# Kernel tuning notes

Hardware: AMD Instinct MI355X
Metric: run time of the kernel (lower is better)

## Reference

```python
import jax, jax.numpy as jnp
import numpy as np

NUM_LAYERS = 2      # args.num_layers
EPS = 1e-6          # poincare_to_lorentz eps
NORM_CLIP = 1.0     # exp_map norm_control clip
N, K, F, D = 30000, 32, 256, 128


def _normalize_lorentz(h):
    # project onto hyperboloid: time = sqrt(1 + |space|^2)
    sp = h[:, 1:]
    t = jnp.sqrt(1.0 + jnp.sum(sp * sp, axis=-1, keepdims=True))
    return jnp.concatenate([t, sp], axis=-1)


def _exp_map_zero(v):
    # tangent vector at origin has zero time component (normalize_tan with x=0)
    sp = v[:, 1:]
    ldv = jnp.sum(sp * sp, axis=-1, keepdims=True)          # Lorentz norm^2 of (0, sp)
    nd = jnp.sqrt(jnp.clip(ldv + 1e-9, 1e-10, None))
    t = jnp.minimum(nd, NORM_CLIP)                           # norm_control
    time = jnp.cosh(t)
    space = jnp.sinh(t) * sp / nd
    return _normalize_lorentz(jnp.concatenate([time, space], axis=-1))


def _hyperbolic_mean(nbr, w):
    # nbr: [N, K, D] Lorentz points; w: [N, K] neighbor weights
    k = nbr[..., 1:] / nbr[..., :1]                          # h2k: Klein model
    kn = jnp.clip(jnp.sum(k * k, axis=-1, keepdims=True), 0.0, 0.9)
    lam = w[..., None] / jnp.sqrt(1.0 - kn)                  # weighted Lorentz factors
    k_mean = jnp.sum(lam * k, axis=1) / jnp.sum(lam, axis=1)  # [N, D-1]
    # k2h: Klein -> hyperboloid
    kn2 = jnp.minimum(jnp.sum(k_mean * k_mean, axis=-1, keepdims=True), 0.9)
    ones = jnp.ones((k_mean.shape[0], 1), k_mean.dtype)
    return jnp.concatenate([ones, k_mean], axis=-1) / jnp.sqrt(1.0 - kn2)


def _lorentz_activation(h):
    # lorentz -> poincare, SELU, poincare -> lorentz (c = 1)
    p = h[:, 1:] / (h[:, :1] + 1.0)
    p = jax.nn.selu(p)
    pn = jnp.sum(p * p, axis=-1, keepdims=True)
    return jnp.concatenate([1.0 + pn, 2.0 * p], axis=-1) / (1.0 - pn + EPS)


def setup_inputs() -> dict:
    key = jax.random.key(0)
    k1, k2, k3, k4, k5 = jax.random.split(key, 5)
    x = jax.random.normal(k1, (N, F), dtype=jnp.float32)
    adj = jax.random.randint(k2, (N, K), 0, N, dtype=jnp.int32)
    w = jax.random.uniform(k3, (N, K), dtype=jnp.float32)
    lin_W = jax.random.normal(k4, (F, D), dtype=jnp.float32) / np.sqrt(F)
    lin_b = jnp.zeros((D,), dtype=jnp.float32)
    M, _ = jnp.linalg.qr(jax.random.normal(k5, (D - 1, D - 1), dtype=jnp.float32))  # orthogonal init
    return {"x": x, "adj": adj, "w": w, "lin_W": lin_W, "lin_b": lin_b, "M": M}


def reference(x, adj, w, lin_W, lin_b, M):
    h = jax.nn.selu(x @ lin_W + lin_b)          # Euclidean projection + activation
    h = _exp_map_zero(h)                        # lift to hyperboloid
    d = h.shape[-1]
    # retrieve_params: block-diag [[1,0],[0,M]] Lorentz rotation (tie_weight -> shared)
    lw = jnp.zeros((d, d), h.dtype).at[0, 0].set(1.0).at[1:, 1:].set(M)
    for _ in range(NUM_LAYERS):
        msg = h @ lw                             # Stiefel transform
        nbr = msg[adj]                           # [N, K, D] neighbor gather
        h = _hyperbolic_mean(nbr, w)             # Klein weighted mean
        h = _lorentz_activation(h)               # SELU in Poincare model
        h = _normalize_lorentz(h)                # re-project onto hyperboloid
    return h
```

## Files before the change

kernel.cpp:

```cpp
#include <hip/hip_runtime.h>
#include <hip/hip_fp16.h>
#include <math.h>

#define NN 30000
#define KK 32
#define FF 256
#define DD 128
#define NB 938

typedef _Float16 f16x8 __attribute__((ext_vector_type(8)));
typedef float f32x4v __attribute__((ext_vector_type(4)));

__device__ __forceinline__ float seluf(float x) {
    const float scale = 1.0507009873554804934193349852946f;
    const float alpha = 1.6732632423543772848170429916717f;
    return x > 0.f ? scale * x : scale * alpha * expm1f(x);
}

__device__ __forceinline__ float waveReduceSum(float v) {
#pragma unroll
    for (int m = 1; m < 64; m <<= 1) v += __shfl_xor(v, m, 64);
    return v;
}

__global__ __launch_bounds__(256) void k_prep(
    const float* __restrict__ W, const float* __restrict__ M,
    _Float16* __restrict__ Wt, _Float16* __restrict__ Lt)
{
    const int b = blockIdx.x, t = threadIdx.x;
    if (b < 128) {
        Wt[b * FF + t] = (_Float16)W[t * DD + b];
    } else if (t < 128) {
        const int c = b - 128, k = t;
        const float v = (k == 0 && c == 0) ? 1.f
                      : ((k >= 1 && c >= 1) ? M[(k - 1) * 127 + (c - 1)] : 0.f);
        Lt[c * DD + k] = (_Float16)v;
    }
}

__global__ __launch_bounds__(256) void k_lin_exp(
    const float* __restrict__ x, const _Float16* __restrict__ Wt,
    const float* __restrict__ b, float* __restrict__ h)
{
    __shared__ float red[4][16];
    const int wv_ = threadIdx.x >> 6;
    const int lane = threadIdx.x & 63;
    const int g = lane >> 4, c16 = lane & 15;
    const int baseRow = blockIdx.x * 32 + (wv_ >> 1) * 16;
    const int nb = (wv_ & 1) * 4;
    const int arow = baseRow + c16;
    const bool rowOK = arow < NN;

    float4 f[16];
    const float4* xp = (const float4*)(x + (size_t)arow * FF) + g * 2;
    if (rowOK) {
#pragma unroll
        for (int ks = 0; ks < 8; ++ks) {
            f[2 * ks]     = xp[ks * 8];
            f[2 * ks + 1] = xp[ks * 8 + 1];
        }
    } else {
#pragma unroll
        for (int i = 0; i < 16; ++i) f[i] = float4{0.f, 0.f, 0.f, 0.f};
    }
    f16x8 ahi[8], alo[8];
#pragma unroll
    for (int ks = 0; ks < 8; ++ks) {
        const float q[8] = {f[2 * ks].x, f[2 * ks].y, f[2 * ks].z, f[2 * ks].w,
                            f[2 * ks + 1].x, f[2 * ks + 1].y, f[2 * ks + 1].z, f[2 * ks + 1].w};
#pragma unroll
        for (int j = 0; j < 8; ++j) {
            ahi[ks][j] = (_Float16)q[j];
            alo[ks][j] = (_Float16)(q[j] - (float)ahi[ks][j]);
        }
    }

    f32x4v acc[4];
#pragma unroll
    for (int n = 0; n < 4; ++n) acc[n] = f32x4v{0.f, 0.f, 0.f, 0.f};
#pragma unroll
    for (int ks = 0; ks < 8; ++ks) {
#pragma unroll
        for (int n = 0; n < 4; ++n) {
            const f16x8 bh = *(const f16x8*)(Wt + (size_t)((nb + n) * 16 + c16) * FF + ks * 32 + g * 8);
            acc[n] = __builtin_amdgcn_mfma_f32_16x16x32_f16(ahi[ks], bh, acc[n], 0, 0, 0);
            acc[n] = __builtin_amdgcn_mfma_f32_16x16x32_f16(alo[ks], bh, acc[n], 0, 0, 0);
        }
    }

    float bias[4];
#pragma unroll
    for (int n = 0; n < 4; ++n) bias[n] = b[(nb + n) * 16 + c16];

    float vv[4][4];
#pragma unroll
    for (int r = 0; r < 4; ++r) {
        float part = 0.f;
#pragma unroll
        for (int n = 0; n < 4; ++n) {
            vv[r][n] = seluf(acc[n][r] + bias[n]);
            float sq = vv[r][n] * vv[r][n];
            if (nb == 0 && n == 0 && c16 == 0) sq = 0.f;
            part += sq;
        }
#pragma unroll
        for (int m = 1; m < 16; m <<= 1) part += __shfl_xor(part, m, 64);
        if (c16 == 0) red[wv_][4 * g + r] = part;
    }
    __syncthreads();
#pragma unroll
    for (int r = 0; r < 4; ++r) {
        const int row = baseRow + 4 * g + r;
        const float ldv = red[wv_][4 * g + r] + red[wv_ ^ 1][4 * g + r];
        const float nd = sqrtf(fmaxf(ldv + 1e-9f, 1e-10f));
        const float t  = fminf(nd, 1.0f);
        const float sc = sinhf(t) / nd;
        const float tm = sqrtf(1.f + sc * sc * ldv);
        if (row < NN) {
#pragma unroll
            for (int n = 0; n < 4; ++n) {
                const float o = (nb == 0 && n == 0 && c16 == 0) ? tm : sc * vv[r][n];
                h[(size_t)row * DD + (nb + n) * 16 + c16] = o;
            }
        }
    }
}

__global__ __launch_bounds__(256) void k_msg_aux(
    const float* __restrict__ h, const _Float16* __restrict__ Lt,
    __half* __restrict__ table)
{
    __shared__ float red[4][16];
    __shared__ float m0s[2][16];
    const int wv_ = threadIdx.x >> 6;
    const int lane = threadIdx.x & 63;
    const int g = lane >> 4, c16 = lane & 15;
    const int baseRow = blockIdx.x * 32 + (wv_ >> 1) * 16;
    const int nb = (wv_ & 1) * 4;
    const int arow = baseRow + c16;
    const bool rowOK = arow < NN;

    float4 f[8];
    const float4* hp = (const float4*)(h + (size_t)arow * DD) + g * 2;
    if (rowOK) {
#pragma unroll
        for (int ks = 0; ks < 4; ++ks) {
            f[2 * ks]     = hp[ks * 8];
            f[2 * ks + 1] = hp[ks * 8 + 1];
        }
    } else {
#pragma unroll
        for (int i = 0; i < 8; ++i) f[i] = float4{0.f, 0.f, 0.f, 0.f};
    }
    f16x8 ahi[4], alo[4];
#pragma unroll
    for (int ks = 0; ks < 4; ++ks) {
        const float q[8] = {f[2 * ks].x, f[2 * ks].y, f[2 * ks].z, f[2 * ks].w,
                            f[2 * ks + 1].x, f[2 * ks + 1].y, f[2 * ks + 1].z, f[2 * ks + 1].w};
#pragma unroll
        for (int j = 0; j < 8; ++j) {
            ahi[ks][j] = (_Float16)q[j];
            alo[ks][j] = (_Float16)(q[j] - (float)ahi[ks][j]);
        }
    }

    f32x4v acc[4];
#pragma unroll
    for (int n = 0; n < 4; ++n) acc[n] = f32x4v{0.f, 0.f, 0.f, 0.f};
#pragma unroll
    for (int ks = 0; ks < 4; ++ks) {
#pragma unroll
        for (int n = 0; n < 4; ++n) {
            const f16x8 bh = *(const f16x8*)(Lt + (size_t)((nb + n) * 16 + c16) * DD + ks * 32 + g * 8);
            acc[n] = __builtin_amdgcn_mfma_f32_16x16x32_f16(ahi[ks], bh, acc[n], 0, 0, 0);
            acc[n] = __builtin_amdgcn_mfma_f32_16x16x32_f16(alo[ks], bh, acc[n], 0, 0, 0);
        }
    }

#pragma unroll
    for (int r = 0; r < 4; ++r) {
        float part = 0.f;
#pragma unroll
        for (int n = 0; n < 4; ++n) {
            float sq = acc[n][r] * acc[n][r];
            if (nb == 0 && n == 0 && c16 == 0) sq = 0.f;
            part += sq;
        }
#pragma unroll
        for (int m = 1; m < 16; m <<= 1) part += __shfl_xor(part, m, 64);
        if (c16 == 0) red[wv_][4 * g + r] = part;
        if (nb == 0 && c16 == 0) m0s[wv_ >> 1][4 * g + r] = acc[0][r];
    }
    __syncthreads();
#pragma unroll
    for (int r = 0; r < 4; ++r) {
        const int row = baseRow + 4 * g + r;
        const float rn = 1.f / m0s[wv_ >> 1][4 * g + r];
        const float sum2 = red[wv_][4 * g + r] + red[wv_ ^ 1][4 * g + r];
        float kn = sum2 * rn * rn;
        kn = fminf(fmaxf(kn, 0.f), 0.9f);
        const float fh = 1.f / sqrtf(1.f - kn);
        if (row < NN) {
#pragma unroll
            for (int n = 0; n < 4; ++n) {
                const float val = (nb == 0 && n == 0 && c16 == 0) ? fh : acc[n][r] * rn;
                table[(size_t)row * DD + (nb + n) * 16 + c16] = __float2half(val);
            }
        }
    }
}

__global__ __launch_bounds__(256) void k_layer(
    const __half* __restrict__ table, const int* __restrict__ adj,
    const float* __restrict__ w, float* __restrict__ out)
{
    const int wave = threadIdx.x >> 6;
    const int lane = threadIdx.x & 63;
    const int node = blockIdx.x * 4 + wave;

    const int   av = adj[node * KK + (lane & 31)];
    const float wv = w[node * KK + (lane & 31)];

    unsigned int vbits[32];
#pragma unroll
    for (int j = 0; j < KK; ++j) {
        const int idx = __shfl(av, j, 64);
        vbits[j] = *(const unsigned int*)(table + (size_t)idx * DD + lane * 2);
    }

    const float f  = __half2float(table[(size_t)av * DD]);
    const float lam = wv * f;
    float ls = lam;
#pragma unroll
    for (int m = 1; m < 32; m <<= 1) ls += __shfl_xor(ls, m, 64);

    float km0 = 0.f, km1 = 0.f;
#pragma unroll
    for (int j = 0; j < KK; ++j) {
        const float cj = __shfl(lam, j, 64);
        const __half2 hh = *(const __half2*)&vbits[j];
        const float2 v = __half22float2(hh);
        km0 = fmaf(cj, v.x, km0);
        km1 = fmaf(cj, v.y, km1);
    }
    const float rl = 1.f / ls;
    const float m0 = km0 * rl;
    const float m1 = km1 * rl;
    float c2 = (lane ? m0 * m0 : 0.f) + m1 * m1;
    const float kn2 = fminf(waveReduceSum(c2), 0.9f);
    const float invs = 1.f / sqrtf(1.f - kn2);
    const float pd = invs + 1.f;
    const float p0 = lane ? seluf(m0 * invs / pd) : 0.f;
    const float p1 = seluf(m1 * invs / pd);
    float pc = p0 * p0 + p1 * p1;
    const float pn = waveReduceSum(pc);
    const float rdn = 1.f / (1.f - pn + 1e-6f);
    const float tm = sqrtf(1.f + 4.f * pn * rdn * rdn);
    float2 o;
    o.x = lane ? 2.f * p0 * rdn : tm;
    o.y = 2.f * p1 * rdn;
    *(float2*)(out + (size_t)node * DD + lane * 2) = o;
}

extern "C" void kernel_launch(void* const* d_in, const int* in_sizes, int n_in,
                              void* d_out, int out_size, void* d_ws, size_t ws_size,
                              hipStream_t stream) {
    const float* x     = (const float*)d_in[0];
    const int*   adj   = (const int*)d_in[1];
    const float* w     = (const float*)d_in[2];
    const float* lin_W = (const float*)d_in[3];
    const float* lin_b = (const float*)d_in[4];
    const float* M     = (const float*)d_in[5];
    float*  h     = (float*)d_out;
    char*   ws    = (char*)d_ws;
    __half* table = (__half*)ws;
    _Float16* Wt  = (_Float16*)(ws + 7680000);
    _Float16* Lt  = (_Float16*)(ws + 7745536);

    k_prep<<<256, 256, 0, stream>>>(lin_W, M, Wt, Lt);
    k_lin_exp<<<NB, 256, 0, stream>>>(x, Wt, lin_b, h);
    k_msg_aux<<<NB, 256, 0, stream>>>(h, Lt, table);
    k_layer<<<NN / 4, 256, 0, stream>>>(table, adj, w, h);
    k_msg_aux<<<NB, 256, 0, stream>>>(h, Lt, table);
    k_layer<<<NN / 4, 256, 0, stream>>>(table, adj, w, h);
}
```

Before: 132.8 us.

## Split neighbor-gather layer kernel into two column-half passes with staged partials

The gather/aggregate layer kernel becomes two kernels. Each one gathers only half of every neighbor row (64 fp16 columns), with the intent of shrinking the per-pass gathered working set so it stays resident in cache. The first pass writes partial means, the neighbor weights, the weight sum and a partial squared norm to workspace. The second pass reads these back to finish the normalization and activation. In exchange there are extra launches, the adj indices are read twice, partial results round-trip through global memory, and each gather is now a 2-byte-per-lane load, which is narrower.

```diff
diff --git a/kernel.cpp b/kernel.cpp
--- a/kernel.cpp
+++ b/kernel.cpp
@@ -210,9 +210,10 @@
     }
 }
 
-__global__ __launch_bounds__(256) void k_layer(
+__global__ __launch_bounds__(256) void k_layer_a(
     const __half* __restrict__ table, const int* __restrict__ adj,
-    const float* __restrict__ w, float* __restrict__ out)
+    const float* __restrict__ w, float* __restrict__ mA,
+    float* __restrict__ lamW, float2* __restrict__ hdr)
 {
     const int wave = threadIdx.x >> 6;
     const int lane = threadIdx.x & 63;
@@ -221,45 +222,73 @@
     const int   av = adj[node * KK + (lane & 31)];
     const float wv = w[node * KK + (lane & 31)];
 
-    unsigned int vbits[32];
+    const unsigned short* tb = (const unsigned short*)table;
+    unsigned short vb[KK];
 #pragma unroll
     for (int j = 0; j < KK; ++j) {
         const int idx = __shfl(av, j, 64);
-        vbits[j] = *(const unsigned int*)(table + (size_t)idx * DD + lane * 2);
-    }
-
-    const float f  = __half2float(table[(size_t)av * DD]);
+        vb[j] = tb[(size_t)idx * DD + lane];
+    }
+    const float f = __half2float(table[(size_t)av * DD]);
     const float lam = wv * f;
     float ls = lam;
 #pragma unroll
     for (int m = 1; m < 32; m <<= 1) ls += __shfl_xor(ls, m, 64);
 
-    float km0 = 0.f, km1 = 0.f;
+    float km = 0.f;
 #pragma unroll
     for (int j = 0; j < KK; ++j) {
         const float cj = __shfl(lam, j, 64);
-        const __half2 hh = *(const __half2*)&vbits[j];
-        const float2 v = __half22float2(hh);
-        km0 = fmaf(cj, v.x, km0);
-        km1 = fmaf(cj, v.y, km1);
+        km = fmaf(cj, __half2float(*(const __half*)&vb[j]), km);
     }
     const float rl = 1.f / ls;
-    const float m0 = km0 * rl;
-    const float m1 = km1 * rl;
-    float c2 = (lane ? m0 * m0 : 0.f) + m1 * m1;
-    const float kn2 = fminf(waveReduceSum(c2), 0.9f);
+    const float m_ = km * rl;
+    const float c2 = waveReduceSum(lane ? m_ * m_ : 0.f);
+    mA[(size_t)node * 64 + lane] = m_;
+    if (lane < KK) lamW[(size_t)node * KK + lane] = lam;
+    if (lane == 0) hdr[node] = float2{ls, c2};
+}
+
+__global__ __launch_bounds__(256) void k_layer_b(
+    const __half* __restrict__ table, const int* __restrict__ adj,
+    const float* __restrict__ mA, const float* __restrict__ lamW,
+    const float2* __restrict__ hdr, float* __restrict__ out)
+{
+    const int wave = threadIdx.x >> 6;
+    const int lane = threadIdx.x & 63;
+    const int node = blockIdx.x * 4 + wave;
+
+    const int av = adj[node * KK + (lane & 31)];
+    const unsigned short* tb = (const unsigned short*)table;
+    unsigned short vb[KK];
+#pragma unroll
+    for (int j = 0; j < KK; ++j) {
+        const int idx = __shfl(av, j, 64);
+        vb[j] = tb[(size_t)idx * DD + 64 + lane];
+    }
+    const float lam = lamW[(size_t)node * KK + (lane & 31)];
+
+    float km = 0.f;
+#pragma unroll
+    for (int j = 0; j < KK; ++j) {
+        const float cj = __shfl(lam, j, 64);
+        km = fmaf(cj, __half2float(*(const __half*)&vb[j]), km);
+    }
+    const float2 hd = hdr[node];
+    const float rl = 1.f / hd.x;
+    const float mB = km * rl;
+    const float c2B = waveReduceSum(mB * mB);
+    const float kn2 = fminf(hd.y + c2B, 0.9f);
     const float invs = 1.f / sqrtf(1.f - kn2);
     const float pd = invs + 1.f;
-    const float p0 = lane ? seluf(m0 * invs / pd) : 0.f;
-    const float p1 = seluf(m1 * invs / pd);
-    float pc = p0 * p0 + p1 * p1;
-    const float pn = waveReduceSum(pc);
+    const float mAv = mA[(size_t)node * 64 + lane];
+    const float pA = lane ? seluf(mAv * invs / pd) : 0.f;
+    const float pB = seluf(mB * invs / pd);
+    const float pn = waveReduceSum(pA * pA + pB * pB);
     const float rdn = 1.f / (1.f - pn + 1e-6f);
     const float tm = sqrtf(1.f + 4.f * pn * rdn * rdn);
-    float2 o;
-    o.x = lane ? 2.f * p0 * rdn : tm;
-    o.y = 2.f * p1 * rdn;
-    *(float2*)(out + (size_t)node * DD + lane * 2) = o;
+    out[(size_t)node * DD + lane]      = lane ? 2.f * pA * rdn : tm;
+    out[(size_t)node * DD + 64 + lane] = 2.f * pB * rdn;
 }
 
 extern "C" void kernel_launch(void* const* d_in, const int* in_sizes, int n_in,
@@ -273,14 +302,19 @@
     const float* M     = (const float*)d_in[5];
     float*  h     = (float*)d_out;
     char*   ws    = (char*)d_ws;
-    __half* table = (__half*)ws;
-    _Float16* Wt  = (_Float16*)(ws + 7680000);
-    _Float16* Lt  = (_Float16*)(ws + 7745536);
+    __half*   table = (__half*)ws;
+    _Float16* Wt    = (_Float16*)(ws + 7680000);
+    _Float16* Lt    = (_Float16*)(ws + 7745536);
+    float*    mA    = (float*)(ws + 7778304);
+    float*    lamW  = (float*)(ws + 15458304);
+    float2*   hdr   = (float2*)(ws + 19298304);
 
     k_prep<<<256, 256, 0, stream>>>(lin_W, M, Wt, Lt);
     k_lin_exp<<<NB, 256, 0, stream>>>(x, Wt, lin_b, h);
     k_msg_aux<<<NB, 256, 0, stream>>>(h, Lt, table);
-    k_layer<<<NN / 4, 256, 0, stream>>>(table, adj, w, h);
+    k_layer_a<<<NN / 4, 256, 0, stream>>>(table, adj, w, mA, lamW, hdr);
+    k_layer_b<<<NN / 4, 256, 0, stream>>>(table, adj, mA, lamW, hdr, h);
     k_msg_aux<<<NB, 256, 0, stream>>>(h, Lt, table);
-    k_layer<<<NN / 4, 256, 0, stream>>>(table, adj, w, h);
-}
+    k_layer_a<<<NN / 4, 256, 0, stream>>>(table, adj, w, mA, lamW, hdr);
+    k_layer_b<<<NN / 4, 256, 0, stream>>>(table, adj, mA, lamW, hdr, h);
+}
```

After: 177.9 us. 34.0% more time.

## Fuse linear+exp-map kernel with first message transform via shared memory

Applied to the files above, without the earlier changes.

Merges the initial projection/exp-map kernel with the first Stiefel-transform/Klein-table kernel. The lifted h tile is staged in LDS instead of being written to and re-read from global memory, which saves one launch and a 15 MB round trip. It also splits the x load into two halves, which may reduce register pressure. The cost is more LDS per block (about 17 KB) and an extra barrier, which could lower occupancy.

```diff
diff --git a/kernel.cpp b/kernel.cpp
--- a/kernel.cpp
+++ b/kernel.cpp
@@ -38,40 +38,48 @@
     }
 }
 
-__global__ __launch_bounds__(256) void k_lin_exp(
+__global__ __launch_bounds__(256) void k_lin_exp_msg(
     const float* __restrict__ x, const _Float16* __restrict__ Wt,
-    const float* __restrict__ b, float* __restrict__ h)
+    const float* __restrict__ b, const _Float16* __restrict__ Lt,
+    __half* __restrict__ table)
 {
+    __shared__ float hs[32][132];
     __shared__ float red[4][16];
+    __shared__ float m0s[2][16];
     const int wv_ = threadIdx.x >> 6;
     const int lane = threadIdx.x & 63;
     const int g = lane >> 4, c16 = lane & 15;
-    const int baseRow = blockIdx.x * 32 + (wv_ >> 1) * 16;
+    const int rowHalf = wv_ >> 1;
+    const int baseRow = blockIdx.x * 32 + rowHalf * 16;
     const int nb = (wv_ & 1) * 4;
     const int arow = baseRow + c16;
     const bool rowOK = arow < NN;
 
-    float4 f[16];
+    f16x8 ahi[8], alo[8];
     const float4* xp = (const float4*)(x + (size_t)arow * FF) + g * 2;
-    if (rowOK) {
-#pragma unroll
-        for (int ks = 0; ks < 8; ++ks) {
-            f[2 * ks]     = xp[ks * 8];
-            f[2 * ks + 1] = xp[ks * 8 + 1];
-        }
-    } else {
-#pragma unroll
-        for (int i = 0; i < 16; ++i) f[i] = float4{0.f, 0.f, 0.f, 0.f};
-    }
-    f16x8 ahi[8], alo[8];
-#pragma unroll
-    for (int ks = 0; ks < 8; ++ks) {
-        const float q[8] = {f[2 * ks].x, f[2 * ks].y, f[2 * ks].z, f[2 * ks].w,
-                            f[2 * ks + 1].x, f[2 * ks + 1].y, f[2 * ks + 1].z, f[2 * ks + 1].w};
-#pragma unroll
-        for (int j = 0; j < 8; ++j) {
-            ahi[ks][j] = (_Float16)q[j];
-            alo[ks][j] = (_Float16)(q[j] - (float)ahi[ks][j]);
+#pragma unroll
+    for (int c = 0; c < 2; ++c) {
+        float4 f[8];
+        if (rowOK) {
+#pragma unroll
+            for (int kk = 0; kk < 4; ++kk) {
+                f[2 * kk]     = xp[(c * 4 + kk) * 8];
+                f[2 * kk + 1] = xp[(c * 4 + kk) * 8 + 1];
+            }
+        } else {
+#pragma unroll
+            for (int i = 0; i < 8; ++i) f[i] = float4{0.f, 0.f, 0.f, 0.f};
+        }
+#pragma unroll
+        for (int kk = 0; kk < 4; ++kk) {
+            const int ks = c * 4 + kk;
+            const float q[8] = {f[2 * kk].x, f[2 * kk].y, f[2 * kk].z, f[2 * kk].w,
+                                f[2 * kk + 1].x, f[2 * kk + 1].y, f[2 * kk + 1].z, f[2 * kk + 1].w};
+#pragma unroll
+            for (int j = 0; j < 8; ++j) {
+                ahi[ks][j] = (_Float16)q[j];
+                alo[ks][j] = (_Float16)(q[j] - (float)ahi[ks][j]);
+            }
         }
     }
 
@@ -110,17 +118,74 @@
     __syncthreads();
 #pragma unroll
     for (int r = 0; r < 4; ++r) {
-        const int row = baseRow + 4 * g + r;
+        const int lrow = rowHalf * 16 + 4 * g + r;
         const float ldv = red[wv_][4 * g + r] + red[wv_ ^ 1][4 * g + r];
         const float nd = sqrtf(fmaxf(ldv + 1e-9f, 1e-10f));
         const float t  = fminf(nd, 1.0f);
         const float sc = sinhf(t) / nd;
         const float tm = sqrtf(1.f + sc * sc * ldv);
+#pragma unroll
+        for (int n = 0; n < 4; ++n) {
+            const float o = (nb == 0 && n == 0 && c16 == 0) ? tm : sc * vv[r][n];
+            hs[lrow][(nb + n) * 16 + c16] = o;
+        }
+    }
+    __syncthreads();
+
+    f16x8 mhi[4], mlo[4];
+#pragma unroll
+    for (int ks = 0; ks < 4; ++ks) {
+        const float* hp = &hs[rowHalf * 16 + c16][ks * 32 + g * 8];
+        const float4 f0 = *(const float4*)hp;
+        const float4 f1 = *(const float4*)(hp + 4);
+        const float q[8] = {f0.x, f0.y, f0.z, f0.w, f1.x, f1.y, f1.z, f1.w};
+#pragma unroll
+        for (int j = 0; j < 8; ++j) {
+            mhi[ks][j] = (_Float16)q[j];
+            mlo[ks][j] = (_Float16)(q[j] - (float)mhi[ks][j]);
+        }
+    }
+
+#pragma unroll
+    for (int n = 0; n < 4; ++n) acc[n] = f32x4v{0.f, 0.f, 0.f, 0.f};
+#pragma unroll
+    for (int ks = 0; ks < 4; ++ks) {
+#pragma unroll
+        for (int n = 0; n < 4; ++n) {
+            const f16x8 bh = *(const f16x8*)(Lt + (size_t)((nb + n) * 16 + c16) * DD + ks * 32 + g * 8);
+            acc[n] = __builtin_amdgcn_mfma_f32_16x16x32_f16(mhi[ks], bh, acc[n], 0, 0, 0);
+            acc[n] = __builtin_amdgcn_mfma_f32_16x16x32_f16(mlo[ks], bh, acc[n], 0, 0, 0);
+        }
+    }
+
+#pragma unroll
+    for (int r = 0; r < 4; ++r) {
+        float part = 0.f;
+#pragma unroll
+        for (int n = 0; n < 4; ++n) {
+            float sq = acc[n][r] * acc[n][r];
+            if (nb == 0 && n == 0 && c16 == 0) sq = 0.f;
+            part += sq;
+        }
+#pragma unroll
+        for (int m = 1; m < 16; m <<= 1) part += __shfl_xor(part, m, 64);
+        if (c16 == 0) red[wv_][4 * g + r] = part;
+        if (nb == 0 && c16 == 0) m0s[rowHalf][4 * g + r] = acc[0][r];
+    }
+    __syncthreads();
+#pragma unroll
+    for (int r = 0; r < 4; ++r) {
+        const int row = baseRow + 4 * g + r;
+        const float rn = 1.f / m0s[rowHalf][4 * g + r];
+        const float sum2 = red[wv_][4 * g + r] + red[wv_ ^ 1][4 * g + r];
+        float kn = sum2 * rn * rn;
+        kn = fminf(fmaxf(kn, 0.f), 0.9f);
+        const float fh = 1.f / sqrtf(1.f - kn);
         if (row < NN) {
 #pragma unroll
             for (int n = 0; n < 4; ++n) {
-                const float o = (nb == 0 && n == 0 && c16 == 0) ? tm : sc * vv[r][n];
-                h[(size_t)row * DD + (nb + n) * 16 + c16] = o;
+                const float val = (nb == 0 && n == 0 && c16 == 0) ? fh : acc[n][r] * rn;
+                table[(size_t)row * DD + (nb + n) * 16 + c16] = __float2half(val);
             }
         }
     }
@@ -273,13 +338,12 @@
     const float* M     = (const float*)d_in[5];
     float*  h     = (float*)d_out;
     char*   ws    = (char*)d_ws;
-    __half* table = (__half*)ws;
-    _Float16* Wt  = (_Float16*)(ws + 7680000);
-    _Float16* Lt  = (_Float16*)(ws + 7745536);
+    __half*   table = (__half*)ws;
+    _Float16* Wt    = (_Float16*)(ws + 7680000);
+    _Float16* Lt    = (_Float16*)(ws + 7745536);
 
     k_prep<<<256, 256, 0, stream>>>(lin_W, M, Wt, Lt);
-    k_lin_exp<<<NB, 256, 0, stream>>>(x, Wt, lin_b, h);
-    k_msg_aux<<<NB, 256, 0, stream>>>(h, Lt, table);
+    k_lin_exp_msg<<<NB, 256, 0, stream>>>(x, Wt, lin_b, Lt, table);
     k_layer<<<NN / 4, 256, 0, stream>>>(table, adj, w, h);
     k_msg_aux<<<NB, 256, 0, stream>>>(h, Lt, table);
     k_layer<<<NN / 4, 256, 0, stream>>>(table, adj, w, h);
```

Result: faster. 124.8 us (-6.0%).
